# Optimization experiments

Hardware: AMD Instinct MI355X
Metric: run time of the kernel (lower is better)

The kernel has to match this reference:

```python
import jax, jax.numpy as jnp
import numpy as np

N, E, G = 50000, 800000, 128
H, NUM_RBF, CUTOFF, TIME_DIM, L = 128, 32, 6.0, 64, 4
MAX_Z, LIGAND_NODE = 128, 1
M_IN = 3 * H + NUM_RBF + 1


def _ln(x, g, b, eps=1e-5):
    mu = x.mean(-1, keepdims=True)
    var = ((x - mu) ** 2).mean(-1, keepdims=True)
    return (x - mu) * jax.lax.rsqrt(var + eps) * g + b


def _sin_emb(t, dim):
    half = dim // 2
    freqs = jnp.exp(jnp.arange(half, dtype=jnp.float32) * (-np.log(10000.0) / (half - 1)))
    args = t[:, None] * freqs[None, :]
    return jnp.concatenate([jnp.sin(args), jnp.cos(args)], axis=-1)


def setup_inputs() -> dict:
    key = jax.random.key(0)
    ks = jax.random.split(key, 32)
    d = {}
    d['z'] = jax.random.randint(ks[0], (N,), 0, MAX_Z)
    d['node_type'] = jax.random.randint(ks[1], (N,), 0, 2)
    d['pos'] = jax.random.normal(ks[2], (N, 3), jnp.float32) * 3.0
    d['edge_index'] = jax.random.randint(ks[3], (2, E), 0, N)
    d['edge_type'] = jax.random.randint(ks[4], (E,), 0, 2)
    d['batch'] = jnp.sort(jax.random.randint(ks[5], (N,), 0, G))
    d['t'] = jax.random.uniform(ks[6], (G,), jnp.float32)

    def lin(k, fi, fo):
        return jax.random.normal(k, (fi, fo), jnp.float32) / np.sqrt(fi)

    d['emb_z'] = jax.random.normal(ks[7], (MAX_Z, H), jnp.float32) * 0.02
    d['emb_nt'] = jax.random.normal(ks[8], (2, H), jnp.float32) * 0.02
    d['in_norm_g'] = jnp.ones((H,), jnp.float32)
    d['in_norm_b'] = jnp.zeros((H,), jnp.float32)
    d['time_w1'] = lin(ks[9], TIME_DIM, H); d['time_b1'] = jnp.zeros((H,), jnp.float32)
    d['time_w2'] = lin(ks[10], H, H); d['time_b2'] = jnp.zeros((H,), jnp.float32)
    d['l_edge_emb'] = jax.random.normal(ks[11], (L, 2, H), jnp.float32) * 0.02
    d['l_msg_w1'] = jax.random.normal(ks[12], (L, M_IN, H), jnp.float32) / np.sqrt(M_IN)
    d['l_msg_b1'] = jnp.zeros((L, H), jnp.float32)
    d['l_msg_w2'] = jax.random.normal(ks[13], (L, H, H), jnp.float32) / np.sqrt(H)
    d['l_msg_b2'] = jnp.zeros((L, H), jnp.float32)
    d['l_upd_w1'] = jax.random.normal(ks[14], (L, 2 * H, H), jnp.float32) / np.sqrt(2 * H)
    d['l_upd_b1'] = jnp.zeros((L, H), jnp.float32)
    d['l_upd_w2'] = jax.random.normal(ks[15], (L, H, H), jnp.float32) / np.sqrt(H)
    d['l_upd_b2'] = jnp.zeros((L, H), jnp.float32)
    d['l_norm_g'] = jnp.ones((L, H), jnp.float32)
    d['l_norm_b'] = jnp.zeros((L, H), jnp.float32)
    d['head_w1'] = lin(ks[16], H, H); d['head_b1'] = jnp.zeros((H,), jnp.float32)
    d['head_w2'] = lin(ks[17], H, 1); d['head_b2'] = jnp.zeros((1,), jnp.float32)
    return d


def reference(z, node_type, pos, edge_index, edge_type, batch, t,
              emb_z, emb_nt, in_norm_g, in_norm_b,
              time_w1, time_b1, time_w2, time_b2,
              l_edge_emb, l_msg_w1, l_msg_b1, l_msg_w2, l_msg_b2,
              l_upd_w1, l_upd_b1, l_upd_w2, l_upd_b2, l_norm_g, l_norm_b,
              head_w1, head_b1, head_w2, head_b2):
    centers = jnp.linspace(0.0, CUTOFF, NUM_RBF)
    step = CUTOFF / (NUM_RBF - 1)
    gamma = 1.0 / max(step * step, 1e-6)

    h = emb_z[jnp.clip(z, 0, MAX_Z - 1)] + emb_nt[node_type]
    tf = jax.nn.silu(_sin_emb(t, TIME_DIM) @ time_w1 + time_b1) @ time_w2 + time_b2
    h = h + tf[batch]
    h = _ln(h, in_norm_g, in_norm_b)

    src, dst = edge_index[0], edge_index[1]
    rel = pos[src] - pos[dst]                     # [E,3]
    dist = jnp.linalg.norm(rel, axis=-1)          # [E]
    radial = jnp.exp(-gamma * (dist[:, None] - centers[None, :]) ** 2)  # [E,R]
    lig = node_type == LIGAND_NODE

    for i in range(L):
        ek = l_edge_emb[i][edge_type]             # [E,H]
        m_in = jnp.concatenate([h[src], h[dst], ek, radial, dist[:, None]], axis=-1)
        msg = jax.nn.silu(m_in @ l_msg_w1[i] + l_msg_b1[i])
        msg = jax.nn.silu(msg @ l_msg_w2[i] + l_msg_b2[i])
        sums = jax.ops.segment_sum(msg, dst, num_segments=N)
        cnt = jax.ops.segment_sum(jnp.ones((E,), h.dtype), dst, num_segments=N)
        agg = sums / jnp.clip(cnt, 1.0)[:, None]
        upd = jax.nn.silu(jnp.concatenate([h, agg], axis=-1) @ l_upd_w1[i] + l_upd_b1[i])
        upd = upd @ l_upd_w2[i] + l_upd_b2[i]
        h = jnp.where(lig[:, None], _ln(h + upd, l_norm_g[i], l_norm_b[i]), h)

    mask = lig.astype(h.dtype)
    gsum = jax.ops.segment_sum(h * mask[:, None], batch, num_segments=G)
    gcnt = jax.ops.segment_sum(mask, batch, num_segments=G)
    gf = gsum / jnp.clip(gcnt, 1.0)[:, None]
    out = jax.nn.silu(gf @ head_w1 + head_b1) @ head_w2 + head_b2
    return out.squeeze(-1)
```

## Files before the change

### kernel.cpp

```cpp
#include <hip/hip_runtime.h>
#include <hip/hip_bf16.h>

#define NN 50000
#define EE 800000
#define GG 128
#define HH 128
#define XPB 136

typedef __bf16 bf16;
typedef __attribute__((ext_vector_type(8))) __bf16 bf16x8;
typedef __attribute__((ext_vector_type(4))) float f32x4;

__device__ __forceinline__ float silu_f(float x) { return x / (1.0f + __expf(-x)); }

__global__ void prep_weights(const float* __restrict__ w1, const float* __restrict__ w2,
                             const float* __restrict__ u1, const float* __restrict__ u2,
                             const float* __restrict__ ee, const float* __restrict__ mb1,
                             bf16* __restrict__ W1abt, bf16* __restrict__ W1rt,
                             bf16* __restrict__ W2t, bf16* __restrict__ U1t,
                             bf16* __restrict__ U2t) {
    int idx = blockIdx.x * 256 + threadIdx.x;
    if (idx < 131072) {
        int l = idx >> 15, rem = idx & 32767;
        int c = rem >> 7, k = rem & 127;
        int krow = k + ((c >= 128) ? 128 : 0);
        W1abt[idx] = (bf16)w1[(size_t)l * 417 * 128 + (size_t)krow * 128 + (c & 127)];
    } else if ((idx -= 131072) < 32768) {
        int l = idx >> 13, rem = idx & 8191;
        int c = rem >> 6, k = rem & 63;
        const float* w1l = w1 + (size_t)l * 417 * 128;
        float v = 0.0f;
        if (k < 32) v = w1l[(size_t)(384 + k) * 128 + c];
        else if (k == 32) v = w1l[(size_t)416 * 128 + c];
        else if (k == 33) {
            v = mb1[l * 128 + c];
            for (int t = 0; t < 128; ++t)
                v += ee[(size_t)l * 256 + t] * w1l[(size_t)(256 + t) * 128 + c];
        } else if (k == 34) {
            for (int t = 0; t < 128; ++t)
                v += (ee[(size_t)l * 256 + 128 + t] - ee[(size_t)l * 256 + t]) *
                     w1l[(size_t)(256 + t) * 128 + c];
        }
        W1rt[idx] = (bf16)v;
    } else if ((idx -= 32768) < 65536) {
        int l = idx / 16384, rem = idx % 16384;
        int n = rem / 128, k = rem % 128;
        W2t[idx] = (bf16)w2[(size_t)l * 16384 + (size_t)k * 128 + n];
    } else if ((idx -= 65536) < 131072) {
        int l = idx / 32768, rem = idx % 32768;
        int n = rem / 256, k = rem % 256;
        U1t[idx] = (bf16)u1[(size_t)l * 32768 + (size_t)k * 128 + n];
    } else if ((idx -= 131072) < 65536) {
        int l = idx / 16384, rem = idx % 16384;
        int n = rem / 128, k = rem % 128;
        U2t[idx] = (bf16)u2[(size_t)l * 16384 + (size_t)k * 128 + n];
    }
}

__global__ void time_mlp(const float* __restrict__ t, const float* __restrict__ w1,
                         const float* __restrict__ b1, const float* __restrict__ w2,
                         const float* __restrict__ b2, float* __restrict__ tf) {
    int g = blockIdx.x, c = threadIdx.x;
    __shared__ float sL[64], uT[128];
    float tv = t[g];
    if (c < 32) {
        float fr = expf(-(float)c * (logf(10000.0f) / 31.0f));
        float arg = tv * fr;
        sL[c] = sinf(arg);
        sL[c + 32] = cosf(arg);
    }
    __syncthreads();
    float acc = b1[c];
    for (int k = 0; k < 64; ++k) acc += sL[k] * w1[k * 128 + c];
    uT[c] = silu_f(acc);
    __syncthreads();
    float acc2 = b2[c];
    for (int k = 0; k < 128; ++k) acc2 += uT[k] * w2[k * 128 + c];
    tf[g * 128 + c] = acc2;
}

__global__ void node_init(const int* __restrict__ z, const int* __restrict__ nt,
                          const int* __restrict__ batch, const float* __restrict__ tf,
                          const float* __restrict__ emb_z, const float* __restrict__ emb_nt,
                          const float* __restrict__ g, const float* __restrict__ b,
                          float* __restrict__ hg, bf16* __restrict__ hb) {
    int n = blockIdx.x, c = threadIdx.x;
    __shared__ float red[128];
    int zz = min(max(z[n], 0), 127);
    float v = emb_z[zz * 128 + c] + emb_nt[nt[n] * 128 + c] + tf[batch[n] * 128 + c];
    red[c] = v;
    __syncthreads();
    for (int s = 64; s > 0; s >>= 1) { if (c < s) red[c] += red[c + s]; __syncthreads(); }
    float mu = red[0] * (1.0f / 128.0f);
    __syncthreads();
    float dv = v - mu;
    red[c] = dv * dv;
    __syncthreads();
    for (int s = 64; s > 0; s >>= 1) { if (c < s) red[c] += red[c + s]; __syncthreads(); }
    float var = red[0] * (1.0f / 128.0f);
    float o = dv * rsqrtf(var + 1e-5f) * g[c] + b[c];
    hg[(size_t)n * 128 + c] = o;
    hb[(size_t)n * 128 + c] = (bf16)o;
}

__global__ void edge_pre(const int* __restrict__ ei, const float* __restrict__ pos,
                         float* __restrict__ dist_raw, int* __restrict__ cnt) {
    int e = blockIdx.x * 256 + threadIdx.x;
    if (e >= EE) return;
    int s = ei[e], d = ei[EE + e];
    float dx = pos[s * 3 + 0] - pos[d * 3 + 0];
    float dy = pos[s * 3 + 1] - pos[d * 3 + 1];
    float dz = pos[s * 3 + 2] - pos[d * 3 + 2];
    dist_raw[e] = sqrtf(dx * dx + dy * dy + dz * dz);
    atomicAdd(&cnt[d], 1);
}

__global__ void scan_kernel(const int* __restrict__ cnt, int* __restrict__ cursor) {
    __shared__ int part[1024];
    int t = threadIdx.x;
    const int per = (NN + 1023) / 1024;
    int start = t * per, end = min(start + per, NN);
    int s = 0;
    for (int i = start; i < end; ++i) s += cnt[i];
    part[t] = s;
    __syncthreads();
    for (int off = 1; off < 1024; off <<= 1) {
        int v = (t >= off) ? part[t - off] : 0;
        __syncthreads();
        part[t] += v;
        __syncthreads();
    }
    int base = (t == 0) ? 0 : part[t - 1];
    for (int i = start; i < end; ++i) { cursor[i] = base; base += cnt[i]; }
}

__global__ void scatter_kernel(const int* __restrict__ ei, const int* __restrict__ et,
                               const float* __restrict__ dist_raw, int* __restrict__ cursor,
                               int* __restrict__ src_s, int* __restrict__ dst_s,
                               int* __restrict__ type_s, float* __restrict__ dist_s) {
    int e = blockIdx.x * 256 + threadIdx.x;
    if (e >= EE) return;
    int d = ei[EE + e];
    int p = atomicAdd(&cursor[d], 1);
    src_s[p] = ei[e];
    dst_s[p] = d;
    type_s[p] = et[e];
    dist_s[p] = dist_raw[e];
}

__global__ __launch_bounds__(256) void node_pre(
    const bf16* __restrict__ hb, const bf16* __restrict__ W1abt,
    bf16* __restrict__ Xsb, bf16* __restrict__ Xdb) {
    __shared__ bf16 xL[64 * 128];
    const int tid = threadIdx.x;
    const int lane = tid & 63, wave = tid >> 6;
    const int wr = wave >> 1, wc = wave & 1;
    const int lrow = lane & 15, lgrp = lane >> 4;
    const int nb0 = blockIdx.x * 64;
    const int r0 = wr * 32 + lrow, r1 = r0 + 16;

    for (int i = tid; i < 64 * 16; i += 256) {
        const int row = i >> 4, cc = i & 15;
        const int node = nb0 + row;
        bf16x8 v;
        if (node < NN) v = *(const bf16x8*)(hb + (size_t)node * 128 + cc * 8);
        else { for (int j = 0; j < 8; ++j) v[j] = (bf16)0.0f; }
        *(bf16x8*)(xL + row * 128 + ((cc ^ (row & 15)) * 8)) = v;
    }
    __syncthreads();

    f32x4 acc[2][8] = {};
    for (int ks = 0; ks < 4; ++ks) {
        const int cb = ks * 4 + lgrp;
        bf16x8 a0 = *(const bf16x8*)(xL + r0 * 128 + ((cb ^ (r0 & 15)) * 8));
        bf16x8 a1 = *(const bf16x8*)(xL + r1 * 128 + ((cb ^ (r1 & 15)) * 8));
        const int k0 = ks * 32 + lgrp * 8;
#pragma unroll
        for (int ni = 0; ni < 8; ++ni) {
            const int col = wc * 128 + ni * 16 + lrow;
            bf16x8 b = *(const bf16x8*)(W1abt + (size_t)col * 128 + k0);
            acc[0][ni] = __builtin_amdgcn_mfma_f32_16x16x32_bf16(a0, b, acc[0][ni], 0, 0, 0);
            acc[1][ni] = __builtin_amdgcn_mfma_f32_16x16x32_bf16(a1, b, acc[1][ni], 0, 0, 0);
        }
    }
#pragma unroll
    for (int mi = 0; mi < 2; ++mi) {
#pragma unroll
        for (int r = 0; r < 4; ++r) {
            const int row = wr * 32 + mi * 16 + lgrp * 4 + r;
            const int node = nb0 + row;
            if (node >= NN) continue;
#pragma unroll
            for (int ni = 0; ni < 8; ++ni) {
                const int col = wc * 128 + ni * 16 + lrow;
                float v = (mi == 0 ? acc[0][ni][r] : acc[1][ni][r]);
                if (col < 128) Xsb[(size_t)node * 128 + col] = (bf16)v;
                else Xdb[(size_t)node * 128 + (col - 128)] = (bf16)v;
            }
        }
    }
}

__global__ __launch_bounds__(256) void edge_kernel(
    const int* __restrict__ src_s, const int* __restrict__ dst_s,
    const int* __restrict__ type_s, const float* __restrict__ dist_s,
    const bf16* __restrict__ Xsb, const bf16* __restrict__ Xdb,
    const bf16* __restrict__ W1rt, const bf16* __restrict__ W2t,
    const float* __restrict__ b2, float* __restrict__ sums) {
    __shared__ bf16 xbL[64 * XPB];
    __shared__ bf16 msgL[64 * 128];
    __shared__ int dstL[64];
    __shared__ int srcL[64];
    const int tid = threadIdx.x;
    const int lane = tid & 63, wave = tid >> 6;
    const int wr = wave >> 1, wc = wave & 1;
    const int lrow = lane & 15, lgrp = lane >> 4;
    const int eb = blockIdx.x * 64;

    const int r0 = wr * 32 + lrow;
    const int r1 = r0 + 16;
    const int e0 = eb + r0, e1 = eb + r1;
    const int ty0 = type_s[e0], ty1 = type_s[e1];
    const float di0 = dist_s[e0], di1 = dist_s[e1];
    if (tid < 64) { dstL[tid] = dst_s[eb + tid]; srcL[tid] = src_s[eb + tid]; }
    __syncthreads();

#pragma unroll
    for (int i = tid; i < 64 * 16; i += 256) {
        const int row = i >> 4, c8 = (i & 15) << 3;
        bf16x8 a = *(const bf16x8*)(Xsb + (size_t)srcL[row] * 128 + c8);
        bf16x8 b = *(const bf16x8*)(Xdb + (size_t)dstL[row] * 128 + c8);
        bf16x8 s;
#pragma unroll
        for (int j = 0; j < 8; ++j) s[j] = (bf16)((float)a[j] + (float)b[j]);
        *(bf16x8*)(xbL + row * XPB + c8) = s;
    }

    const float step = 6.0f / 31.0f;
    const float gamma = 1.0f / (step * step);

    f32x4 acc[2][4] = {};
#pragma unroll
    for (int ks = 0; ks < 2; ++ks) {
        const int k0 = ks * 32 + lgrp * 8;
        bf16x8 a0, a1;
        if (k0 < 32) {
#pragma unroll
            for (int j = 0; j < 8; ++j) {
                float cj = (float)(k0 + j) * step;
                float v0 = di0 - cj, v1 = di1 - cj;
                a0[j] = (bf16)__expf(-gamma * v0 * v0);
                a1[j] = (bf16)__expf(-gamma * v1 * v1);
            }
        } else {
#pragma unroll
            for (int j = 0; j < 8; ++j) { a0[j] = (bf16)0.0f; a1[j] = (bf16)0.0f; }
            if (k0 == 32) {
                a0[0] = (bf16)di0; a1[0] = (bf16)di1;
                a0[1] = (bf16)1.0f; a1[1] = (bf16)1.0f;
                a0[2] = (bf16)(float)ty0; a1[2] = (bf16)(float)ty1;
            }
        }
#pragma unroll
        for (int ni = 0; ni < 4; ++ni) {
            const int col = wc * 64 + ni * 16 + lrow;
            bf16x8 b = *(const bf16x8*)(W1rt + (size_t)col * 64 + k0);
            acc[0][ni] = __builtin_amdgcn_mfma_f32_16x16x32_bf16(a0, b, acc[0][ni], 0, 0, 0);
            acc[1][ni] = __builtin_amdgcn_mfma_f32_16x16x32_bf16(a1, b, acc[1][ni], 0, 0, 0);
        }
    }
    __syncthreads();

#pragma unroll
    for (int mi = 0; mi < 2; ++mi) {
#pragma unroll
        for (int r = 0; r < 4; ++r) {
            const int row = wr * 32 + mi * 16 + lgrp * 4 + r;
            const bf16* xr = xbL + row * XPB;
#pragma unroll
            for (int ni = 0; ni < 4; ++ni) {
                const int col = wc * 64 + ni * 16 + lrow;
                float v = (mi == 0 ? acc[0][ni][r] : acc[1][ni][r]) + (float)xr[col];
                v = silu_f(v);
                const int cc = col >> 3;
                msgL[row * 128 + ((cc ^ (row & 15)) * 8) + (col & 7)] = (bf16)v;
            }
        }
    }
    __syncthreads();

    f32x4 acc2[2][4] = {};
#pragma unroll
    for (int ks = 0; ks < 4; ++ks) {
        const int cb = ks * 4 + lgrp;
        bf16x8 a0 = *(const bf16x8*)(msgL + r0 * 128 + ((cb ^ (r0 & 15)) * 8));
        bf16x8 a1 = *(const bf16x8*)(msgL + r1 * 128 + ((cb ^ (r1 & 15)) * 8));
        const int k0 = ks * 32 + lgrp * 8;
#pragma unroll
        for (int ni = 0; ni < 4; ++ni) {
            const int col = wc * 64 + ni * 16 + lrow;
            bf16x8 b = *(const bf16x8*)(W2t + (size_t)col * 128 + k0);
            acc2[0][ni] = __builtin_amdgcn_mfma_f32_16x16x32_bf16(a0, b, acc2[0][ni], 0, 0, 0);
            acc2[1][ni] = __builtin_amdgcn_mfma_f32_16x16x32_bf16(a1, b, acc2[1][ni], 0, 0, 0);
        }
    }
#pragma unroll
    for (int mi = 0; mi < 2; ++mi) {
#pragma unroll
        for (int ni = 0; ni < 4; ++ni) {
            const int col = wc * 64 + ni * 16 + lrow;
            const float bias = b2[col];
#pragma unroll
            for (int r = 0; r < 4; ++r) {
                const int row = wr * 32 + mi * 16 + lgrp * 4 + r;
                float v = silu_f((mi == 0 ? acc2[0][ni][r] : acc2[1][ni][r]) + bias);
                xbL[row * XPB + col] = (bf16)v;
            }
        }
    }
    __syncthreads();
    {
        const int cp = (tid & 63) * 2;
        const int q = tid >> 6;
        float a0s = 0.0f, a1s = 0.0f;
        int cur = dstL[q * 16];
        for (int i = 0; i < 16; ++i) {
            const int row = q * 16 + i;
            const int dd = dstL[row];
            if (dd != cur) {
                atomicAdd(&sums[(size_t)cur * 128 + cp], a0s);
                atomicAdd(&sums[(size_t)cur * 128 + cp + 1], a1s);
                a0s = 0.0f; a1s = 0.0f; cur = dd;
            }
            const unsigned u = *(const unsigned*)(xbL + row * XPB + cp);
            a0s += __uint_as_float(u << 16);
            a1s += __uint_as_float(u & 0xffff0000u);
        }
        atomicAdd(&sums[(size_t)cur * 128 + cp], a0s);
        atomicAdd(&sums[(size_t)cur * 128 + cp + 1], a1s);
    }
}

__global__ __launch_bounds__(256) void node_kernel(
    float* __restrict__ hg, bf16* __restrict__ hb, const float* __restrict__ sums,
    const int* __restrict__ cnt, const int* __restrict__ node_type,
    const bf16* __restrict__ U1t, const bf16* __restrict__ U2t,
    const float* __restrict__ ub1, const float* __restrict__ ub2,
    const float* __restrict__ ng, const float* __restrict__ nb_) {
    __shared__ char smem[49152];
    bf16* xL = (bf16*)smem;
    bf16* uL = (bf16*)(smem + 32768);
    float* u2f = (float*)smem;
    const int tid = threadIdx.x;
    const int lane = tid & 63, wave = tid >> 6;
    const int wr = wave >> 1, wc = wave & 1;
    const int lrow = lane & 15, lgrp = lane >> 4;
    const int nb0 = blockIdx.x * 64;
    const int r0 = wr * 32 + lrow, r1 = r0 + 16;

    for (int i = tid; i < 64 * 32; i += 256) {
        const int row = i >> 5, cc = i & 31;
        const int node = nb0 + row;
        bf16x8 v;
        if (node < NN) {
            const int col8 = cc * 8;
            if (col8 < 128) {
                v = *(const bf16x8*)(hb + (size_t)node * 128 + col8);
            } else {
                const float inv = 1.0f / fmaxf((float)cnt[node], 1.0f);
                const float4 f0 = *(const float4*)(sums + (size_t)node * 128 + (col8 - 128));
                const float4 f1 = *(const float4*)(sums + (size_t)node * 128 + (col8 - 128) + 4);
                v[0] = (bf16)(f0.x * inv); v[1] = (bf16)(f0.y * inv);
                v[2] = (bf16)(f0.z * inv); v[3] = (bf16)(f0.w * inv);
                v[4] = (bf16)(f1.x * inv); v[5] = (bf16)(f1.y * inv);
                v[6] = (bf16)(f1.z * inv); v[7] = (bf16)(f1.w * inv);
            }
        } else {
#pragma unroll
            for (int j = 0; j < 8; ++j) v[j] = (bf16)0.0f;
        }
        *(bf16x8*)(xL + row * 256 + ((cc ^ (row & 15)) * 8)) = v;
    }
    __syncthreads();

    f32x4 acc[2][4] = {};
    for (int ks = 0; ks < 8; ++ks) {
        const int cb = ks * 4 + lgrp;
        bf16x8 a0 = *(const bf16x8*)(xL + r0 * 256 + ((cb ^ (r0 & 15)) * 8));
        bf16x8 a1 = *(const bf16x8*)(xL + r1 * 256 + ((cb ^ (r1 & 15)) * 8));
        const int k0 = ks * 32 + lgrp * 8;
#pragma unroll
        for (int ni = 0; ni < 4; ++ni) {
            const int col = wc * 64 + ni * 16 + lrow;
            bf16x8 b = *(const bf16x8*)(U1t + (size_t)col * 256 + k0);
            acc[0][ni] = __builtin_amdgcn_mfma_f32_16x16x32_bf16(a0, b, acc[0][ni], 0, 0, 0);
            acc[1][ni] = __builtin_amdgcn_mfma_f32_16x16x32_bf16(a1, b, acc[1][ni], 0, 0, 0);
        }
    }
#pragma unroll
    for (int mi = 0; mi < 2; ++mi) {
#pragma unroll
        for (int ni = 0; ni < 4; ++ni) {
            const int col = wc * 64 + ni * 16 + lrow;
            const float bias = ub1[col];
            const int cc = col >> 3;
#pragma unroll
            for (int r = 0; r < 4; ++r) {
                const int row = wr * 32 + mi * 16 + lgrp * 4 + r;
                float v = silu_f((mi == 0 ? acc[0][ni][r] : acc[1][ni][r]) + bias);
                uL[row * 128 + ((cc ^ (row & 15)) * 8) + (col & 7)] = (bf16)v;
            }
        }
    }
    __syncthreads();

    f32x4 acc2[2][4] = {};
    for (int ks = 0; ks < 4; ++ks) {
        const int cb = ks * 4 + lgrp;
        bf16x8 a0 = *(const bf16x8*)(uL + r0 * 128 + ((cb ^ (r0 & 15)) * 8));
        bf16x8 a1 = *(const bf16x8*)(uL + r1 * 128 + ((cb ^ (r1 & 15)) * 8));
        const int k0 = ks * 32 + lgrp * 8;
#pragma unroll
        for (int ni = 0; ni < 4; ++ni) {
            const int col = wc * 64 + ni * 16 + lrow;
            bf16x8 b = *(const bf16x8*)(U2t + (size_t)col * 128 + k0);
            acc2[0][ni] = __builtin_amdgcn_mfma_f32_16x16x32_bf16(a0, b, acc2[0][ni], 0, 0, 0);
            acc2[1][ni] = __builtin_amdgcn_mfma_f32_16x16x32_bf16(a1, b, acc2[1][ni], 0, 0, 0);
        }
    }
    __syncthreads();
#pragma unroll
    for (int mi = 0; mi < 2; ++mi) {
#pragma unroll
        for (int ni = 0; ni < 4; ++ni) {
            const int col = wc * 64 + ni * 16 + lrow;
            const float bias = ub2[col];
#pragma unroll
            for (int r = 0; r < 4; ++r) {
                const int row = wr * 32 + mi * 16 + lgrp * 4 + r;
                u2f[row * 129 + col] = (mi == 0 ? acc2[0][ni][r] : acc2[1][ni][r]) + bias;
            }
        }
    }
    __syncthreads();
    if (tid < 64) {
        const int node = nb0 + tid;
        if (node < NN && node_type[node] == 1) {
            float sum = 0.0f, sq = 0.0f;
            for (int c = 0; c < 128; ++c) {
                float s = hg[(size_t)node * 128 + c] + u2f[tid * 129 + c];
                sum += s; sq += s * s;
            }
            float mu = sum * (1.0f / 128.0f);
            float var = sq * (1.0f / 128.0f) - mu * mu;
            float rstd = rsqrtf(var + 1e-5f);
            for (int c = 0; c < 128; ++c) {
                float s = hg[(size_t)node * 128 + c] + u2f[tid * 129 + c];
                float o = (s - mu) * rstd * ng[c] + nb_[c];
                hg[(size_t)node * 128 + c] = o;
                hb[(size_t)node * 128 + c] = (bf16)o;
            }
        }
    }
}

__global__ void pool_kernel(const int* __restrict__ nt, const int* __restrict__ batch,
                            const float* __restrict__ hg, float* __restrict__ gsum,
                            float* __restrict__ gcnt) {
    int idx = blockIdx.x * 256 + threadIdx.x;
    int n = idx >> 7, c = idx & 127;
    if (n >= NN) return;
    if (nt[n] == 1) {
        int b = batch[n];
        atomicAdd(&gsum[b * 128 + c], hg[(size_t)n * 128 + c]);
        if (c == 0) atomicAdd(&gcnt[b], 1.0f);
    }
}

__global__ void head_kernel(const float* __restrict__ gsum, const float* __restrict__ gcnt,
                            const float* __restrict__ w1, const float* __restrict__ b1,
                            const float* __restrict__ w2, const float* __restrict__ b2,
                            float* __restrict__ out) {
    int g = blockIdx.x, c = threadIdx.x;
    __shared__ float gfL[128], uH[128];
    float inv = 1.0f / fmaxf(gcnt[g], 1.0f);
    gfL[c] = gsum[g * 128 + c] * inv;
    __syncthreads();
    float acc = b1[c];
    for (int k = 0; k < 128; ++k) acc += gfL[k] * w1[k * 128 + c];
    uH[c] = silu_f(acc);
    __syncthreads();
    gfL[c] = uH[c] * w2[c];
    __syncthreads();
    for (int s = 64; s > 0; s >>= 1) { if (c < s) gfL[c] += gfL[c + s]; __syncthreads(); }
    if (c == 0) out[g] = gfL[0] + b2[0];
}

extern "C" void kernel_launch(void* const* d_in, const int* in_sizes, int n_in,
                              void* d_out, int out_size, void* d_ws, size_t ws_size,
                              hipStream_t stream) {
    const int* z = (const int*)d_in[0];
    const int* node_type = (const int*)d_in[1];
    const float* pos = (const float*)d_in[2];
    const int* edge_index = (const int*)d_in[3];
    const int* edge_type = (const int*)d_in[4];
    const int* batch = (const int*)d_in[5];
    const float* t_in = (const float*)d_in[6];
    const float* emb_z = (const float*)d_in[7];
    const float* emb_nt = (const float*)d_in[8];
    const float* in_norm_g = (const float*)d_in[9];
    const float* in_norm_b = (const float*)d_in[10];
    const float* time_w1 = (const float*)d_in[11];
    const float* time_b1 = (const float*)d_in[12];
    const float* time_w2 = (const float*)d_in[13];
    const float* time_b2 = (const float*)d_in[14];
    const float* l_edge_emb = (const float*)d_in[15];
    const float* l_msg_w1 = (const float*)d_in[16];
    const float* l_msg_b1 = (const float*)d_in[17];
    const float* l_msg_w2 = (const float*)d_in[18];
    const float* l_msg_b2 = (const float*)d_in[19];
    const float* l_upd_w1 = (const float*)d_in[20];
    const float* l_upd_b1 = (const float*)d_in[21];
    const float* l_upd_w2 = (const float*)d_in[22];
    const float* l_upd_b2 = (const float*)d_in[23];
    const float* l_norm_g = (const float*)d_in[24];
    const float* l_norm_b = (const float*)d_in[25];
    const float* head_w1 = (const float*)d_in[26];
    const float* head_b1 = (const float*)d_in[27];
    const float* head_w2 = (const float*)d_in[28];
    const float* head_b2 = (const float*)d_in[29];
    float* out = (float*)d_out;

    char* w = (char*)d_ws;
    auto alloc = [&](size_t bytes) {
        char* p = w;
        w += (bytes + 255) & ~(size_t)255;
        return p;
    };
    float* hg = (float*)alloc((size_t)NN * 128 * 4);
    bf16* hb = (bf16*)alloc((size_t)NN * 128 * 2);
    float* sums = (float*)alloc((size_t)NN * 128 * 4);
    bf16* Xsb = (bf16*)alloc((size_t)NN * 128 * 2);
    bf16* Xdb = (bf16*)alloc((size_t)NN * 128 * 2);
    int* cnt = (int*)alloc((size_t)NN * 4);
    int* cursor = (int*)alloc((size_t)NN * 4);
    int* src_s = (int*)alloc((size_t)EE * 4);
    int* dst_s = (int*)alloc((size_t)EE * 4);
    int* type_s = (int*)alloc((size_t)EE * 4);
    float* dist_s = (float*)alloc((size_t)EE * 4);
    float* dist_raw = (float*)alloc((size_t)EE * 4);
    bf16* W1abt = (bf16*)alloc((size_t)4 * 256 * 128 * 2);
    bf16* W1rt = (bf16*)alloc((size_t)4 * 128 * 64 * 2);
    bf16* W2t = (bf16*)alloc((size_t)4 * 128 * 128 * 2);
    bf16* U1t = (bf16*)alloc((size_t)4 * 128 * 256 * 2);
    bf16* U2t = (bf16*)alloc((size_t)4 * 128 * 128 * 2);
    float* tf = (float*)alloc((size_t)GG * 128 * 4);
    float* gsum = (float*)alloc((size_t)GG * 128 * 4);
    float* gcnt = (float*)alloc((size_t)GG * 4);

    hipMemsetAsync(cnt, 0, (size_t)NN * 4, stream);
    prep_weights<<<1664, 256, 0, stream>>>(l_msg_w1, l_msg_w2, l_upd_w1, l_upd_w2,
                                           l_edge_emb, l_msg_b1, W1abt, W1rt, W2t, U1t, U2t);
    time_mlp<<<GG, 128, 0, stream>>>(t_in, time_w1, time_b1, time_w2, time_b2, tf);
    node_init<<<NN, 128, 0, stream>>>(z, node_type, batch, tf, emb_z, emb_nt,
                                      in_norm_g, in_norm_b, hg, hb);
    edge_pre<<<(EE + 255) / 256, 256, 0, stream>>>(edge_index, pos, dist_raw, cnt);
    scan_kernel<<<1, 1024, 0, stream>>>(cnt, cursor);
    scatter_kernel<<<(EE + 255) / 256, 256, 0, stream>>>(edge_index, edge_type, dist_raw,
                                                         cursor, src_s, dst_s, type_s, dist_s);
    for (int l = 0; l < 4; ++l) {
        node_pre<<<(NN + 63) / 64, 256, 0, stream>>>(hb, W1abt + (size_t)l * 32768, Xsb, Xdb);
        hipMemsetAsync(sums, 0, (size_t)NN * 128 * 4, stream);
        edge_kernel<<<EE / 64, 256, 0, stream>>>(
            src_s, dst_s, type_s, dist_s, Xsb, Xdb, W1rt + (size_t)l * 8192,
            W2t + (size_t)l * 16384, l_msg_b2 + l * 128, sums);
        node_kernel<<<(NN + 63) / 64, 256, 0, stream>>>(
            hg, hb, sums, cnt, node_type, U1t + (size_t)l * 32768, U2t + (size_t)l * 16384,
            l_upd_b1 + l * 128, l_upd_b2 + l * 128, l_norm_g + l * 128, l_norm_b + l * 128);
    }
    hipMemsetAsync(gsum, 0, (size_t)GG * 128 * 4, stream);
    hipMemsetAsync(gcnt, 0, (size_t)GG * 4, stream);
    pool_kernel<<<(NN * 128 + 255) / 256, 256, 0, stream>>>(node_type, batch, hg, gsum, gcnt);
    head_kernel<<<GG, 128, 0, stream>>>(gsum, gcnt, head_w1, head_b1, head_w2, head_b2, out);
}
```

Before: 1.456 ms.

## Parallelize node LayerNorm, fuse sums zeroing into node kernel, restructure edge LDS

The node kernel's LayerNorm now uses four threads per node with shuffle reductions instead of one thread per node over 128 columns. The aggregated sums are zeroed by the node kernel after reading, which removes the per-layer memset. The edge kernel stores gathered source and destination features separately in swizzled LDS and adds them in the epilogue, reusing those buffers in place of the message buffer. This adds extra LDS reads and a barrier, and relies on every sums entry being read and cleared.

Result: slower. 1.603 ms (+10.1%).

```diff
diff --git a/kernel.cpp b/kernel.cpp
--- a/kernel.cpp
+++ b/kernel.cpp
@@ -5,7 +5,6 @@
 #define EE 800000
 #define GG 128
 #define HH 128
-#define XPB 136
 
 typedef __bf16 bf16;
 typedef __attribute__((ext_vector_type(8))) __bf16 bf16x8;
@@ -207,8 +206,8 @@
     const bf16* __restrict__ Xsb, const bf16* __restrict__ Xdb,
     const bf16* __restrict__ W1rt, const bf16* __restrict__ W2t,
     const float* __restrict__ b2, float* __restrict__ sums) {
-    __shared__ bf16 xbL[64 * XPB];
-    __shared__ bf16 msgL[64 * 128];
+    __shared__ bf16 xsL[64 * 128];
+    __shared__ bf16 xdL[64 * 128];
     __shared__ int dstL[64];
     __shared__ int srcL[64];
     const int tid = threadIdx.x;
@@ -226,14 +225,14 @@
     __syncthreads();
 
 #pragma unroll
-    for (int i = tid; i < 64 * 16; i += 256) {
-        const int row = i >> 4, c8 = (i & 15) << 3;
-        bf16x8 a = *(const bf16x8*)(Xsb + (size_t)srcL[row] * 128 + c8);
-        bf16x8 b = *(const bf16x8*)(Xdb + (size_t)dstL[row] * 128 + c8);
-        bf16x8 s;
-#pragma unroll
-        for (int j = 0; j < 8; ++j) s[j] = (bf16)((float)a[j] + (float)b[j]);
-        *(bf16x8*)(xbL + row * XPB + c8) = s;
+    for (int it = 0; it < 4; ++it) {
+        const int ci = tid + it * 256;
+        const int row = ci >> 4, cc = ci & 15;
+        const int ccs = (cc ^ (row & 15)) << 3;
+        bf16x8 vs = *(const bf16x8*)(Xsb + (size_t)srcL[row] * 128 + ccs);
+        bf16x8 vd = *(const bf16x8*)(Xdb + (size_t)dstL[row] * 128 + ccs);
+        *(bf16x8*)(xsL + ci * 8) = vs;
+        *(bf16x8*)(xdL + ci * 8) = vd;
     }
 
     const float step = 6.0f / 31.0f;
@@ -276,14 +275,31 @@
 #pragma unroll
         for (int r = 0; r < 4; ++r) {
             const int row = wr * 32 + mi * 16 + lgrp * 4 + r;
-            const bf16* xr = xbL + row * XPB;
+            const int base = row * 128, sw = row & 15;
 #pragma unroll
             for (int ni = 0; ni < 4; ++ni) {
                 const int col = wc * 64 + ni * 16 + lrow;
-                float v = (mi == 0 ? acc[0][ni][r] : acc[1][ni][r]) + (float)xr[col];
-                v = silu_f(v);
-                const int cc = col >> 3;
-                msgL[row * 128 + ((cc ^ (row & 15)) * 8) + (col & 7)] = (bf16)v;
+                const int idx = base + (((col >> 3) ^ sw) << 3) + (col & 7);
+                float v = (mi == 0 ? acc[0][ni][r] : acc[1][ni][r]) +
+                          (float)xsL[idx] + (float)xdL[idx];
+                if (mi == 0) acc[0][ni][r] = silu_f(v);
+                else acc[1][ni][r] = silu_f(v);
+            }
+        }
+    }
+    __syncthreads();
+
+#pragma unroll
+    for (int mi = 0; mi < 2; ++mi) {
+#pragma unroll
+        for (int r = 0; r < 4; ++r) {
+            const int row = wr * 32 + mi * 16 + lgrp * 4 + r;
+            const int base = row * 128, sw = row & 15;
+#pragma unroll
+            for (int ni = 0; ni < 4; ++ni) {
+                const int col = wc * 64 + ni * 16 + lrow;
+                const int idx = base + (((col >> 3) ^ sw) << 3) + (col & 7);
+                xsL[idx] = (bf16)(mi == 0 ? acc[0][ni][r] : acc[1][ni][r]);
             }
         }
     }
@@ -293,8 +309,8 @@
 #pragma unroll
     for (int ks = 0; ks < 4; ++ks) {
         const int cb = ks * 4 + lgrp;
-        bf16x8 a0 = *(const bf16x8*)(msgL + r0 * 128 + ((cb ^ (r0 & 15)) * 8));
-        bf16x8 a1 = *(const bf16x8*)(msgL + r1 * 128 + ((cb ^ (r1 & 15)) * 8));
+        bf16x8 a0 = *(const bf16x8*)(xsL + r0 * 128 + ((cb ^ (r0 & 15)) * 8));
+        bf16x8 a1 = *(const bf16x8*)(xsL + r1 * 128 + ((cb ^ (r1 & 15)) * 8));
         const int k0 = ks * 32 + lgrp * 8;
 #pragma unroll
         for (int ni = 0; ni < 4; ++ni) {
@@ -314,7 +330,7 @@
             for (int r = 0; r < 4; ++r) {
                 const int row = wr * 32 + mi * 16 + lgrp * 4 + r;
                 float v = silu_f((mi == 0 ? acc2[0][ni][r] : acc2[1][ni][r]) + bias);
-                xbL[row * XPB + col] = (bf16)v;
+                xdL[row * 128 + col] = (bf16)v;
             }
         }
     }
@@ -332,7 +348,7 @@
                 atomicAdd(&sums[(size_t)cur * 128 + cp + 1], a1s);
                 a0s = 0.0f; a1s = 0.0f; cur = dd;
             }
-            const unsigned u = *(const unsigned*)(xbL + row * XPB + cp);
+            const unsigned u = *(const unsigned*)(xdL + row * 128 + cp);
             a0s += __uint_as_float(u << 16);
             a1s += __uint_as_float(u & 0xffff0000u);
         }
@@ -342,7 +358,7 @@
 }
 
 __global__ __launch_bounds__(256) void node_kernel(
-    float* __restrict__ hg, bf16* __restrict__ hb, const float* __restrict__ sums,
+    float* __restrict__ hg, bf16* __restrict__ hb, float* __restrict__ sums,
     const int* __restrict__ cnt, const int* __restrict__ node_type,
     const bf16* __restrict__ U1t, const bf16* __restrict__ U2t,
     const float* __restrict__ ub1, const float* __restrict__ ub2,
@@ -368,12 +384,16 @@
                 v = *(const bf16x8*)(hb + (size_t)node * 128 + col8);
             } else {
                 const float inv = 1.0f / fmaxf((float)cnt[node], 1.0f);
-                const float4 f0 = *(const float4*)(sums + (size_t)node * 128 + (col8 - 128));
-                const float4 f1 = *(const float4*)(sums + (size_t)node * 128 + (col8 - 128) + 4);
+                float4* p0 = (float4*)(sums + (size_t)node * 128 + (col8 - 128));
+                float4* p1 = (float4*)(sums + (size_t)node * 128 + (col8 - 128) + 4);
+                const float4 f0 = *p0;
+                const float4 f1 = *p1;
                 v[0] = (bf16)(f0.x * inv); v[1] = (bf16)(f0.y * inv);
                 v[2] = (bf16)(f0.z * inv); v[3] = (bf16)(f0.w * inv);
                 v[4] = (bf16)(f1.x * inv); v[5] = (bf16)(f1.y * inv);
                 v[6] = (bf16)(f1.z * inv); v[7] = (bf16)(f1.w * inv);
+                *p0 = make_float4(0.f, 0.f, 0.f, 0.f);
+                *p1 = make_float4(0.f, 0.f, 0.f, 0.f);
             }
         } else {
 #pragma unroll
@@ -443,19 +463,30 @@
         }
     }
     __syncthreads();
-    if (tid < 64) {
-        const int node = nb0 + tid;
-        if (node < NN && node_type[node] == 1) {
-            float sum = 0.0f, sq = 0.0f;
-            for (int c = 0; c < 128; ++c) {
-                float s = hg[(size_t)node * 128 + c] + u2f[tid * 129 + c];
+    {
+        const int row = tid >> 2, sl = tid & 3;
+        const int node = nb0 + row;
+        const bool lig = (node < NN) && (node_type[node] == 1);
+        float sum = 0.0f, sq = 0.0f;
+        if (lig) {
+#pragma unroll
+            for (int k = 0; k < 32; ++k) {
+                const int c = sl + (k << 2);
+                float s = hg[(size_t)node * 128 + c] + u2f[row * 129 + c];
+                u2f[row * 129 + c] = s;
                 sum += s; sq += s * s;
             }
-            float mu = sum * (1.0f / 128.0f);
-            float var = sq * (1.0f / 128.0f) - mu * mu;
-            float rstd = rsqrtf(var + 1e-5f);
-            for (int c = 0; c < 128; ++c) {
-                float s = hg[(size_t)node * 128 + c] + u2f[tid * 129 + c];
+        }
+        sum += __shfl_xor(sum, 1); sq += __shfl_xor(sq, 1);
+        sum += __shfl_xor(sum, 2); sq += __shfl_xor(sq, 2);
+        if (lig) {
+            const float mu = sum * (1.0f / 128.0f);
+            const float var = sq * (1.0f / 128.0f) - mu * mu;
+            const float rstd = rsqrtf(var + 1e-5f);
+#pragma unroll
+            for (int k = 0; k < 32; ++k) {
+                const int c = sl + (k << 2);
+                float s = u2f[row * 129 + c];
                 float o = (s - mu) * rstd * ng[c] + nb_[c];
                 hg[(size_t)node * 128 + c] = o;
                 hb[(size_t)node * 128 + c] = (bf16)o;
@@ -559,6 +590,7 @@
     float* gcnt = (float*)alloc((size_t)GG * 4);
 
     hipMemsetAsync(cnt, 0, (size_t)NN * 4, stream);
+    hipMemsetAsync(sums, 0, (size_t)NN * 128 * 4, stream);
     prep_weights<<<1664, 256, 0, stream>>>(l_msg_w1, l_msg_w2, l_upd_w1, l_upd_w2,
                                            l_edge_emb, l_msg_b1, W1abt, W1rt, W2t, U1t, U2t);
     time_mlp<<<GG, 128, 0, stream>>>(t_in, time_w1, time_b1, time_w2, time_b2, tf);
@@ -570,7 +602,6 @@
                                                          cursor, src_s, dst_s, type_s, dist_s);
     for (int l = 0; l < 4; ++l) {
         node_pre<<<(NN + 63) / 64, 256, 0, stream>>>(hb, W1abt + (size_t)l * 32768, Xsb, Xdb);
-        hipMemsetAsync(sums, 0, (size_t)NN * 128 * 4, stream);
         edge_kernel<<<EE / 64, 256, 0, stream>>>(
             src_s, dst_s, type_s, dist_s, Xsb, Xdb, W1rt + (size_t)l * 8192,
             W2t + (size_t)l * 16384, l_msg_b2 + l * 128, sums);
```
